# Kernel optimization log

Measured on AMD Instinct MI355X. Metric: run time of the kernel, lower is better.

## Reference

```python
import jax, jax.numpy as jnp
import numpy as np

N, H2, T = 64, 1024, 512  # num steps/documents, 2*hidden_dim, tokens per step
EPS = 1e-12  # torch F.normalize eps


def setup_inputs() -> dict:
    key = jax.random.key(0)
    k1, k2, k3, k4 = jax.random.split(key, 4)
    return {
        "hidden_states": jax.random.normal(k1, (N, H2, T), dtype=jnp.float32),
        "W_attention": jax.random.normal(k2, (H2, H2), dtype=jnp.float32),
        "bias_attention": jax.random.normal(k3, (H2,), dtype=jnp.float32),
        "u_w0": jax.random.normal(k4, (H2,), dtype=jnp.float32),
    }


def reference(hidden_states, W_attention, bias_attention, u_w0):
    n = hidden_states.shape[0]

    # Sequential recurrence on u_w: u_w <- normalize(u_w @ W^T + b), updated
    # BEFORE being used at each step i. Collect the post-update value per step.
    def step(u, _):
        u_new = u @ W_attention.T + bias_attention
        u_new = u_new / jnp.maximum(jnp.linalg.norm(u_new), EPS)
        return u_new, u_new

    _, u_ws = jax.lax.scan(step, u_w0, None, length=n)  # (N, 2H)

    # u_it = tanh(h_i^T W^T + b) for all steps, batched: (N, T, 2H)
    u_it = jnp.tanh(jnp.einsum('ndt,ed->nte', hidden_states, W_attention)
                    + bias_attention)

    # attention scores per step, softmax over the T axis (torch Softmax(dim=0)
    # on a (T,1) column)
    scores = jnp.einsum('nte,ne->nt', u_it, u_ws)  # (N, T)
    a = jax.nn.softmax(scores, axis=1)

    # weighted sum s_i = h_i @ a_i -> stacked as rows: (N, 2H)
    s = jnp.einsum('ndt,nt->nd', hidden_states, a)
    return s
```

## Files before the change

### kernel.cpp

```cpp
#include <hip/hip_runtime.h>
#include <cstdint>
#include <cstddef>

#define H2 1024
#define TT 512
#define NSTEPS 64
#define RBLK 32
#define RTHR 512
#define PREBLK 224
#define TOTBLK (RBLK + PREBLK)

using floatx4 = __attribute__((__ext_vector_type__(4))) float;
using half8   = __attribute__((__ext_vector_type__(8))) _Float16;
using half4   = __attribute__((__ext_vector_type__(4))) _Float16;
typedef unsigned long long u64;

__device__ __forceinline__ float tanh_fast(float x) {
  return 1.0f - 2.0f / (__expf(2.0f * x) + 1.0f);
}

#define GLDS16(gp, lp)                                                         \
  __builtin_amdgcn_global_load_lds(                                            \
      (const __attribute__((address_space(1))) void*)(gp),                     \
      (__attribute__((address_space(3))) void*)(lp), 16, 0, 0)

__global__ __launch_bounds__(RTHR, 1) void recur_pre_kernel(
    const float* __restrict__ W, const float* __restrict__ bias,
    const float* __restrict__ u0, float* __restrict__ vbuf,
    float* __restrict__ norm2, _Float16* __restrict__ Wh,
    const float* __restrict__ h, _Float16* __restrict__ hhT) {
  __shared__ __align__(16) char smem[2 * 16640];
  int tid = threadIdx.x;

  if (blockIdx.x < RBLK) {
    float* ub = (float*)smem;
    float* bredn = (float*)(smem + 8192);
    int w = tid >> 6, l = tid & 63;
    int r0 = blockIdx.x * RBLK + w * 4;

    floatx4 wreg[16];
    float blv[4];
#pragma unroll
    for (int p = 0; p < 4; ++p) {
      const float* wr = W + ((size_t)(r0 + p) << 10) + 4 * l;
#pragma unroll
      for (int j = 0; j < 4; ++j)
        wreg[p * 4 + j] = *(const floatx4*)(wr + 256 * j);
      blv[p] = bias[r0 + p];
    }
#pragma unroll
    for (int j = 0; j < 16; ++j) asm volatile("" : "+v"(wreg[j]));

    for (int i = 0; i < NSTEPS; ++i) {
      float* cb = ub + (i & 1) * 1024;
      float rs;
      if (i == 0) {
        if (w == 0) {
#pragma unroll
          for (int j = 0; j < 4; ++j) {
            floatx4 v = *((const floatx4*)u0 + l + 64 * j);
            *(floatx4*)(cb + 4 * l + 256 * j) = v;
          }
        }
        __syncthreads();
        rs = 1.0f;
      } else {
        if (w == 0) {
          const u64* src = (const u64*)(vbuf + ((size_t)(i - 1) << 10)) + l;
          u64 v[8];
          for (;;) {
            bool ok = true;
#pragma unroll
            for (int j = 0; j < 8; ++j) {
              v[j] = __hip_atomic_load(src + 64 * j, __ATOMIC_RELAXED,
                                       __HIP_MEMORY_SCOPE_AGENT);
              ok &= ((unsigned)(v[j] & 0xFFFFFFFFu) != 0xFFFFFFFFu) &
                    ((unsigned)(v[j] >> 32) != 0xFFFFFFFFu);
            }
            if (__all(ok)) break;
          }
          float sq = 0.f;
#pragma unroll
          for (int j = 0; j < 8; ++j) {
            *(u64*)(cb + 2 * l + 128 * j) = v[j];
            float f0 =
                __builtin_bit_cast(float, (unsigned)(v[j] & 0xFFFFFFFFu));
            float f1 = __builtin_bit_cast(float, (unsigned)(v[j] >> 32));
            sq += f0 * f0 + f1 * f1;
          }
#pragma unroll
          for (int off = 1; off <= 32; off <<= 1)
            sq += __shfl_xor(sq, off, 64);
          if (l == 0) bredn[i & 1] = sq;
        }
        __syncthreads();
        float nrm = bredn[i & 1];
        rs = 1.0f / fmaxf(sqrtf(nrm), 1e-12f);
        if (blockIdx.x == 0 && tid == 64) norm2[i - 1] = nrm;
      }

      float acc0 = 0.f, acc1 = 0.f, acc2 = 0.f, acc3 = 0.f;
#pragma unroll
      for (int j = 0; j < 4; ++j) {
        floatx4 zv = *(const floatx4*)(cb + 256 * j + 4 * l);
        floatx4 w0 = wreg[0 * 4 + j], w1 = wreg[1 * 4 + j];
        floatx4 w2 = wreg[2 * 4 + j], w3 = wreg[3 * 4 + j];
        acc0 += w0.x * zv.x + w0.y * zv.y + w0.z * zv.z + w0.w * zv.w;
        acc1 += w1.x * zv.x + w1.y * zv.y + w1.z * zv.z + w1.w * zv.w;
        acc2 += w2.x * zv.x + w2.y * zv.y + w2.z * zv.z + w2.w * zv.w;
        acc3 += w3.x * zv.x + w3.y * zv.y + w3.z * zv.z + w3.w * zv.w;
      }
#pragma unroll
      for (int off = 1; off <= 32; off <<= 1) {
        acc0 += __shfl_xor(acc0, off, 64);
        acc1 += __shfl_xor(acc1, off, 64);
        acc2 += __shfl_xor(acc2, off, 64);
        acc3 += __shfl_xor(acc3, off, 64);
      }
      if (l == 0) {
        float y0 = acc0 * rs + blv[0], y1 = acc1 * rs + blv[1];
        float y2 = acc2 * rs + blv[2], y3 = acc3 * rs + blv[3];
        u64 a01 = ((u64)__builtin_bit_cast(unsigned, y1) << 32) |
                  (u64)__builtin_bit_cast(unsigned, y0);
        u64 a23 = ((u64)__builtin_bit_cast(unsigned, y3) << 32) |
                  (u64)__builtin_bit_cast(unsigned, y2);
        u64* dst = (u64*)(vbuf + ((size_t)i << 10) + r0);
        __hip_atomic_store(dst, a01, __ATOMIC_RELAXED,
                           __HIP_MEMORY_SCOPE_AGENT);
        __hip_atomic_store(dst + 1, a23, __ATOMIC_RELAXED,
                           __HIP_MEMORY_SCOPE_AGENT);
      }
    }

    if (blockIdx.x == 0 && w == 0) {
      const u64* src = (const u64*)(vbuf + ((size_t)(NSTEPS - 1) << 10)) + l;
      u64 v[8];
      for (;;) {
        bool ok = true;
#pragma unroll
        for (int j = 0; j < 8; ++j) {
          v[j] = __hip_atomic_load(src + 64 * j, __ATOMIC_RELAXED,
                                   __HIP_MEMORY_SCOPE_AGENT);
          ok &= ((unsigned)(v[j] & 0xFFFFFFFFu) != 0xFFFFFFFFu) &
                ((unsigned)(v[j] >> 32) != 0xFFFFFFFFu);
        }
        if (__all(ok)) break;
      }
      float sq = 0.f;
#pragma unroll
      for (int j = 0; j < 8; ++j) {
        float f0 = __builtin_bit_cast(float, (unsigned)(v[j] & 0xFFFFFFFFu));
        float f1 = __builtin_bit_cast(float, (unsigned)(v[j] >> 32));
        sq += f0 * f0 + f1 * f1;
      }
#pragma unroll
      for (int off = 1; off <= 32; off <<= 1) sq += __shfl_xor(sq, off, 64);
      if (l == 0) norm2[NSTEPS - 1] = sq;
    }
  } else {
    int pb = blockIdx.x - RBLK;

    const floatx4* Wv = (const floatx4*)W;
    for (int idx = pb * RTHR + tid; idx < H2 * H2 / 4; idx += PREBLK * RTHR) {
      floatx4 v = Wv[idx];
      half4 o = {(_Float16)v.x, (_Float16)v.y, (_Float16)v.z, (_Float16)v.w};
      ((half4*)Wh)[idx] = o;
    }

    int sub = tid >> 8, ltid = tid & 255;
    float(*tile)[65] = (float(*)[65])(smem + sub * 16640);
    int dr = ltid >> 4, tc = (ltid & 15) << 2;
    int tr = ltid >> 3, seg = ltid & 7;
    for (int base = pb * 2; base < 8192; base += PREBLK * 2) {
      int tidx = base + sub;
      bool act = tidx < 8192;
      int n = tidx >> 7, rem = tidx & 127;
      int d0 = (rem & 15) << 6, t0 = ((rem >> 4) & 7) << 6;
      if (act) {
        const float* hb = h + ((size_t)n * H2 + d0) * TT + t0;
#pragma unroll
        for (int p = 0; p < 4; ++p) {
          floatx4 v = *(const floatx4*)(hb + (size_t)(dr + p * 16) * TT + tc);
          tile[dr + p * 16][tc] = v.x;
          tile[dr + p * 16][tc + 1] = v.y;
          tile[dr + p * 16][tc + 2] = v.z;
          tile[dr + p * 16][tc + 3] = v.w;
        }
      }
      __syncthreads();
      if (act) {
        _Float16* ob = hhT + ((size_t)n * TT + t0) * H2 + d0;
#pragma unroll
        for (int p = 0; p < 2; ++p) {
          int t = tr + p * 32;
          half8 hv;
#pragma unroll
          for (int u = 0; u < 8; ++u) hv[u] = (_Float16)tile[seg * 8 + u][t];
          *(half8*)(ob + (size_t)t * H2 + seg * 8) = hv;
        }
      }
      __syncthreads();
    }
  }
}

__global__ __launch_bounds__(256) void gemm2(
    const _Float16* __restrict__ Wh, const _Float16* __restrict__ hhT,
    const float* __restrict__ bias, const float* __restrict__ vbuf,
    const float* __restrict__ norm2, float* __restrict__ scores) {
  int x = blockIdx.x;
  int xcd = x & 7, slot = x >> 3;
  int e_t = slot & 7;
  int tn = xcd * 32 + (slot >> 3);
  int t_t = tn & 3, n = tn >> 2;
  int e_base = e_t * 128, t_base = t_t * 128;

  int tid = threadIdx.x, lane = tid & 63, w = tid >> 6;
  int q = lane >> 4, m = lane & 15;
  int eoff = (w & 1) * 64, toff = (w >> 1) * 64;

  __shared__ __align__(16) _Float16 Ash[128 * 32];
  __shared__ __align__(16) _Float16 Bsh[128 * 32];

  floatx4 zero = {0.f, 0.f, 0.f, 0.f};
  floatx4 acc[4][4];
#pragma unroll
  for (int i = 0; i < 4; ++i)
#pragma unroll
    for (int j = 0; j < 4; ++j) acc[i][j] = zero;

  int rl = lane >> 2, kseg = lane & 3;
  const _Float16* gA0 =
      Wh + (((size_t)(e_base + w * 32 + rl)) << 10) + kseg * 8;
  const _Float16* gA1 = gA0 + ((size_t)16 << 10);
  const _Float16* gB0 = hhT + ((size_t)n << 19) +
                        (((size_t)(t_base + w * 32 + rl)) << 10) + kseg * 8;
  const _Float16* gB1 = gB0 + ((size_t)16 << 10);
  _Float16* lA0 = Ash + (w * 32) * 32;
  _Float16* lA1 = lA0 + 16 * 32;
  _Float16* lB0 = Bsh + (w * 32) * 32;
  _Float16* lB1 = lB0 + 16 * 32;

  for (int k0 = 0; k0 < H2; k0 += 32) {
    GLDS16(gA0 + k0, lA0);
    GLDS16(gA1 + k0, lA1);
    GLDS16(gB0 + k0, lB0);
    GLDS16(gB1 + k0, lB1);
    __syncthreads();

    half8 af[4], bf[4];
#pragma unroll
    for (int i = 0; i < 4; ++i)
      af[i] = *(const half8*)&Ash[(eoff + i * 16 + m) * 32 + q * 8];
#pragma unroll
    for (int j = 0; j < 4; ++j)
      bf[j] = *(const half8*)&Bsh[(toff + j * 16 + m) * 32 + q * 8];
#pragma unroll
    for (int i = 0; i < 4; ++i)
#pragma unroll
      for (int j = 0; j < 4; ++j)
        acc[i][j] =
            __builtin_amdgcn_mfma_f32_16x16x32_f16(af[i], bf[j], acc[i][j], 0, 0, 0);
    __syncthreads();
  }

  float* uloc = (float*)Ash;
  float* bloc = uloc + 128;
  if (tid < 128) {
    float rsn = 1.0f / fmaxf(sqrtf(norm2[n]), 1e-12f);
    uloc[tid] = vbuf[((size_t)n << 10) + e_base + tid] * rsn;
    bloc[tid] = bias[e_base + tid];
  }
  __syncthreads();

  float part[4] = {0.f, 0.f, 0.f, 0.f};
#pragma unroll
  for (int i = 0; i < 4; ++i) {
#pragma unroll
    for (int reg = 0; reg < 4; ++reg) {
      int el = eoff + i * 16 + q * 4 + reg;
      float ubv = uloc[el];
      float bbv = bloc[el];
#pragma unroll
      for (int j = 0; j < 4; ++j) {
        float y = acc[i][j][reg] + bbv;
        part[j] += tanh_fast(y) * ubv;
      }
    }
  }
#pragma unroll
  for (int j = 0; j < 4; ++j) {
    part[j] += __shfl_xor(part[j], 16, 64);
    part[j] += __shfl_xor(part[j], 32, 64);
    if (lane < 16) {
      int t = t_base + toff + j * 16 + lane;
      atomicAdd(&scores[(size_t)n * TT + t], part[j]);
    }
  }
}

__global__ __launch_bounds__(256) void out_kernel(
    const float* __restrict__ h, const float* __restrict__ scores,
    float* __restrict__ out) {
  int n = blockIdx.y;
  int ds = blockIdx.x;
  int tid = threadIdx.x;
  int w = tid >> 6, lane = tid & 63;

  __shared__ float sa[TT];
  __shared__ float wred[8];

  float s0 = scores[(size_t)n * TT + tid];
  float s1 = scores[(size_t)n * TT + 256 + tid];

  float mx = fmaxf(s0, s1);
#pragma unroll
  for (int off = 32; off >= 1; off >>= 1) mx = fmaxf(mx, __shfl_xor(mx, off, 64));
  if (lane == 0) wred[w] = mx;
  __syncthreads();
  mx = fmaxf(fmaxf(wred[0], wred[1]), fmaxf(wred[2], wred[3]));

  float e0 = __expf(s0 - mx);
  float e1 = __expf(s1 - mx);
  float ssum = e0 + e1;
#pragma unroll
  for (int off = 32; off >= 1; off >>= 1) ssum += __shfl_xor(ssum, off, 64);
  if (lane == 0) wred[4 + w] = ssum;
  __syncthreads();
  ssum = wred[4] + wred[5] + wred[6] + wred[7];
  float inv = 1.0f / ssum;
  sa[tid] = e0 * inv;
  sa[tid + 256] = e1 * inv;
  __syncthreads();

  int d0 = ds * 64 + w * 16;
  const float4* hb = reinterpret_cast<const float4*>(h + (size_t)n * H2 * TT);
#pragma unroll 1
  for (int rr = 0; rr < 16; ++rr) {
    int d = d0 + rr;
    const float4* hr = hb + (size_t)d * (TT / 4);
    float4 a4 = hr[lane];
    float4 b4 = hr[64 + lane];
    int t0 = 4 * lane;
    float acc = a4.x * sa[t0] + a4.y * sa[t0 + 1] + a4.z * sa[t0 + 2] +
                a4.w * sa[t0 + 3] + b4.x * sa[256 + t0] +
                b4.y * sa[256 + t0 + 1] + b4.z * sa[256 + t0 + 2] +
                b4.w * sa[256 + t0 + 3];
#pragma unroll
    for (int off = 1; off <= 32; off <<= 1) acc += __shfl_xor(acc, off, 64);
    if (lane == 0) out[(size_t)n * H2 + d] = acc;
  }
}

extern "C" void kernel_launch(void* const* d_in, const int* in_sizes, int n_in,
                              void* d_out, int out_size, void* d_ws, size_t ws_size,
                              hipStream_t stream) {
  const float* h    = (const float*)d_in[0];
  const float* W    = (const float*)d_in[1];
  const float* bias = (const float*)d_in[2];
  const float* u0   = (const float*)d_in[3];
  float* out = (float*)d_out;

  float* wsf    = (float*)d_ws;
  float* norm2  = wsf;
  float* scores = wsf + 64;
  float* vbuf   = wsf + 64 + NSTEPS * TT;
  unsigned* ctr = (unsigned*)(vbuf + (size_t)NSTEPS * H2);
  float* after_ctr = (float*)(ctr + 16);
  _Float16* Wh  = (_Float16*)after_ctr;
  _Float16* hhT = Wh + (size_t)H2 * H2;

  hipMemsetAsync(d_ws, 0, (size_t)(64 + NSTEPS * TT) * sizeof(float), stream);
  hipMemsetAsync(vbuf, 0xFF, (size_t)NSTEPS * H2 * sizeof(float), stream);

  {
    const float* Wp = W; const float* bp = bias; const float* up = u0;
    float* vp = vbuf; float* np = norm2;
    _Float16* whp = Wh; const float* hp = h; _Float16* htp = hhT;
    void* kargs[] = {&Wp, &bp, &up, &vp, &np, &whp, &hp, &htp};
    hipLaunchCooperativeKernel((void*)recur_pre_kernel, dim3(TOTBLK),
                               dim3(RTHR), kargs, 0, stream);
  }

  gemm2<<<dim3(2048), dim3(256), 0, stream>>>(Wh, hhT, bias, vbuf, norm2,
                                              scores);
  out_kernel<<<dim3(16, 64), dim3(256), 0, stream>>>(h, scores, out);

  (void)in_sizes; (void)n_in; (void)out_size; (void)ws_size;
}
```

Before: 520.7 us.

## Fuse score GEMM into cooperative kernel with dynamic tile queue overlapping recurrence

Folds the separate gemm2 launch into the cooperative recurrence/preprocess kernel. Once all preprocessing blocks signal completion through a counter, all 256 blocks pull GEMM tiles from an atomic work queue, two tiles per 512-thread block. Each tile spin-waits on per-step sentinel values in norm2 and vbuf only at its epilogue, so the GEMM can overlap with the sequential u_w recurrence. This removes one kernel launch and the serialization between recurrence and GEMM. In exchange it adds spin polling, atomic stores for the fp16 conversions, and occupancy limited to the cooperative grid, and the recurrence blocks now share the device with GEMM work.

```diff
diff --git a/kernel.cpp b/kernel.cpp
--- a/kernel.cpp
+++ b/kernel.cpp
@@ -8,7 +8,8 @@
 #define RBLK 32
 #define RTHR 512
 #define PREBLK 224
-#define TOTBLK (RBLK + PREBLK)
+#define TOTBLK 256
+#define NTILES 2048u
 
 using floatx4 = __attribute__((__ext_vector_type__(4))) float;
 using half8   = __attribute__((__ext_vector_type__(8))) _Float16;
@@ -24,13 +25,16 @@
       (const __attribute__((address_space(1))) void*)(gp),                     \
       (__attribute__((address_space(3))) void*)(lp), 16, 0, 0)
 
-__global__ __launch_bounds__(RTHR, 1) void recur_pre_kernel(
+__global__ __launch_bounds__(RTHR, 1) void fused_kernel(
     const float* __restrict__ W, const float* __restrict__ bias,
     const float* __restrict__ u0, float* __restrict__ vbuf,
     float* __restrict__ norm2, _Float16* __restrict__ Wh,
-    const float* __restrict__ h, _Float16* __restrict__ hhT) {
-  __shared__ __align__(16) char smem[2 * 16640];
+    const float* __restrict__ h, _Float16* __restrict__ hhT,
+    float* __restrict__ scores, unsigned* __restrict__ ctrs) {
+  __shared__ __align__(16) char smem[33792];
   int tid = threadIdx.x;
+  unsigned* done  = ctrs;
+  unsigned* queue = ctrs + 16;
 
   if (blockIdx.x < RBLK) {
     float* ub = (float*)smem;
@@ -78,6 +82,7 @@
                     ((unsigned)(v[j] >> 32) != 0xFFFFFFFFu);
             }
             if (__all(ok)) break;
+            __builtin_amdgcn_s_sleep(1);
           }
           float sq = 0.f;
 #pragma unroll
@@ -96,7 +101,11 @@
         __syncthreads();
         float nrm = bredn[i & 1];
         rs = 1.0f / fmaxf(sqrtf(nrm), 1e-12f);
-        if (blockIdx.x == 0 && tid == 64) norm2[i - 1] = nrm;
+        if (blockIdx.x == 0 && tid == 64) {
+          unsigned nb = __builtin_bit_cast(unsigned, nrm);
+          __hip_atomic_store((unsigned*)(norm2 + (i - 1)), nb,
+                             __ATOMIC_RELAXED, __HIP_MEMORY_SCOPE_AGENT);
+        }
       }
 
       float acc0 = 0.f, acc1 = 0.f, acc2 = 0.f, acc3 = 0.f;
@@ -132,8 +141,9 @@
       }
     }
 
-    if (blockIdx.x == 0 && w == 0) {
-      const u64* src = (const u64*)(vbuf + ((size_t)(NSTEPS - 1) << 10)) + l;
+    if (blockIdx.x == 0 && (tid >> 6) == 0) {
+      int l2 = tid & 63;
+      const u64* src = (const u64*)(vbuf + ((size_t)(NSTEPS - 1) << 10)) + l2;
       u64 v[8];
       for (;;) {
         bool ok = true;
@@ -145,6 +155,7 @@
                 ((unsigned)(v[j] >> 32) != 0xFFFFFFFFu);
         }
         if (__all(ok)) break;
+        __builtin_amdgcn_s_sleep(1);
       }
       float sq = 0.f;
 #pragma unroll
@@ -155,8 +166,13 @@
       }
 #pragma unroll
       for (int off = 1; off <= 32; off <<= 1) sq += __shfl_xor(sq, off, 64);
-      if (l == 0) norm2[NSTEPS - 1] = sq;
-    }
+      if (l2 == 0) {
+        unsigned nb = __builtin_bit_cast(unsigned, sq);
+        __hip_atomic_store((unsigned*)(norm2 + (NSTEPS - 1)), nb,
+                           __ATOMIC_RELAXED, __HIP_MEMORY_SCOPE_AGENT);
+      }
+    }
+    __syncthreads();
   } else {
     int pb = blockIdx.x - RBLK;
 
@@ -164,7 +180,8 @@
     for (int idx = pb * RTHR + tid; idx < H2 * H2 / 4; idx += PREBLK * RTHR) {
       floatx4 v = Wv[idx];
       half4 o = {(_Float16)v.x, (_Float16)v.y, (_Float16)v.z, (_Float16)v.w};
-      ((half4*)Wh)[idx] = o;
+      __hip_atomic_store((u64*)Wh + idx, __builtin_bit_cast(u64, o),
+                         __ATOMIC_RELAXED, __HIP_MEMORY_SCOPE_AGENT);
     }
 
     int sub = tid >> 8, ltid = tid & 255;
@@ -193,109 +210,153 @@
 #pragma unroll
         for (int p = 0; p < 2; ++p) {
           int t = tr + p * 32;
-          half8 hv;
-#pragma unroll
-          for (int u = 0; u < 8; ++u) hv[u] = (_Float16)tile[seg * 8 + u][t];
-          *(half8*)(ob + (size_t)t * H2 + seg * 8) = hv;
+          union { half8 v; u64 u[2]; } hu;
+#pragma unroll
+          for (int u = 0; u < 8; ++u) hu.v[u] = (_Float16)tile[seg * 8 + u][t];
+          u64* op = (u64*)(ob + (size_t)t * H2 + seg * 8);
+          __hip_atomic_store(op, hu.u[0], __ATOMIC_RELAXED,
+                             __HIP_MEMORY_SCOPE_AGENT);
+          __hip_atomic_store(op + 1, hu.u[1], __ATOMIC_RELAXED,
+                             __HIP_MEMORY_SCOPE_AGENT);
         }
       }
       __syncthreads();
     }
+    asm volatile("s_waitcnt vmcnt(0)" ::: "memory");
+    __syncthreads();
+    if (tid == 0)
+      __hip_atomic_fetch_add(done, 1u, __ATOMIC_RELEASE,
+                             __HIP_MEMORY_SCOPE_AGENT);
   }
-}
-
-__global__ __launch_bounds__(256) void gemm2(
-    const _Float16* __restrict__ Wh, const _Float16* __restrict__ hhT,
-    const float* __restrict__ bias, const float* __restrict__ vbuf,
-    const float* __restrict__ norm2, float* __restrict__ scores) {
-  int x = blockIdx.x;
-  int xcd = x & 7, slot = x >> 3;
-  int e_t = slot & 7;
-  int tn = xcd * 32 + (slot >> 3);
-  int t_t = tn & 3, n = tn >> 2;
-  int e_base = e_t * 128, t_base = t_t * 128;
-
-  int tid = threadIdx.x, lane = tid & 63, w = tid >> 6;
-  int q = lane >> 4, m = lane & 15;
-  int eoff = (w & 1) * 64, toff = (w >> 1) * 64;
-
-  __shared__ __align__(16) _Float16 Ash[128 * 32];
-  __shared__ __align__(16) _Float16 Bsh[128 * 32];
-
-  floatx4 zero = {0.f, 0.f, 0.f, 0.f};
-  floatx4 acc[4][4];
-#pragma unroll
-  for (int i = 0; i < 4; ++i)
-#pragma unroll
-    for (int j = 0; j < 4; ++j) acc[i][j] = zero;
-
-  int rl = lane >> 2, kseg = lane & 3;
-  const _Float16* gA0 =
-      Wh + (((size_t)(e_base + w * 32 + rl)) << 10) + kseg * 8;
-  const _Float16* gA1 = gA0 + ((size_t)16 << 10);
-  const _Float16* gB0 = hhT + ((size_t)n << 19) +
-                        (((size_t)(t_base + w * 32 + rl)) << 10) + kseg * 8;
-  const _Float16* gB1 = gB0 + ((size_t)16 << 10);
-  _Float16* lA0 = Ash + (w * 32) * 32;
-  _Float16* lA1 = lA0 + 16 * 32;
-  _Float16* lB0 = Bsh + (w * 32) * 32;
-  _Float16* lB1 = lB0 + 16 * 32;
-
-  for (int k0 = 0; k0 < H2; k0 += 32) {
-    GLDS16(gA0 + k0, lA0);
-    GLDS16(gA1 + k0, lA1);
-    GLDS16(gB0 + k0, lB0);
-    GLDS16(gB1 + k0, lB1);
-    __syncthreads();
-
-    half8 af[4], bf[4];
-#pragma unroll
-    for (int i = 0; i < 4; ++i)
-      af[i] = *(const half8*)&Ash[(eoff + i * 16 + m) * 32 + q * 8];
-#pragma unroll
-    for (int j = 0; j < 4; ++j)
-      bf[j] = *(const half8*)&Bsh[(toff + j * 16 + m) * 32 + q * 8];
-#pragma unroll
-    for (int i = 0; i < 4; ++i)
-#pragma unroll
-      for (int j = 0; j < 4; ++j)
-        acc[i][j] =
-            __builtin_amdgcn_mfma_f32_16x16x32_f16(af[i], bf[j], acc[i][j], 0, 0, 0);
-    __syncthreads();
-  }
-
-  float* uloc = (float*)Ash;
-  float* bloc = uloc + 128;
-  if (tid < 128) {
-    float rsn = 1.0f / fmaxf(sqrtf(norm2[n]), 1e-12f);
-    uloc[tid] = vbuf[((size_t)n << 10) + e_base + tid] * rsn;
-    bloc[tid] = bias[e_base + tid];
+
+  if (tid == 0) {
+    while (__hip_atomic_load(done, __ATOMIC_ACQUIRE,
+                             __HIP_MEMORY_SCOPE_AGENT) < (unsigned)PREBLK)
+      __builtin_amdgcn_s_sleep(2);
   }
   __syncthreads();
 
-  float part[4] = {0.f, 0.f, 0.f, 0.f};
-#pragma unroll
-  for (int i = 0; i < 4; ++i) {
-#pragma unroll
-    for (int reg = 0; reg < 4; ++reg) {
-      int el = eoff + i * 16 + q * 4 + reg;
-      float ubv = uloc[el];
-      float bbv = bloc[el];
-#pragma unroll
-      for (int j = 0; j < 4; ++j) {
-        float y = acc[i][j][reg] + bbv;
-        part[j] += tanh_fast(y) * ubv;
-      }
-    }
-  }
-#pragma unroll
-  for (int j = 0; j < 4; ++j) {
-    part[j] += __shfl_xor(part[j], 16, 64);
-    part[j] += __shfl_xor(part[j], 32, 64);
-    if (lane < 16) {
-      int t = t_base + toff + j * 16 + lane;
-      atomicAdd(&scores[(size_t)n * TT + t], part[j]);
-    }
+  int half = tid >> 8, tid2 = tid & 255;
+  _Float16* Ash = (_Float16*)(smem + half * 16384);
+  _Float16* Bsh = Ash + 4096;
+  unsigned* tslot = (unsigned*)(smem + 32768);
+
+  int lane = tid2 & 63, w2 = tid2 >> 6;
+  int q = lane >> 4, m = lane & 15;
+  int eoff = (w2 & 1) * 64, toff = (w2 >> 1) * 64;
+  int rl = lane >> 2, kseg = lane & 3;
+  _Float16* lA0 = Ash + (w2 * 32) * 32;
+  _Float16* lA1 = lA0 + 16 * 32;
+  _Float16* lB0 = Bsh + (w2 * 32) * 32;
+  _Float16* lB1 = lB0 + 16 * 32;
+
+  for (;;) {
+    if (tid == 0) {
+      unsigned q0 = atomicAdd(queue, 2u);
+      tslot[0] = q0;
+      tslot[1] = q0 + 1u;
+    }
+    __syncthreads();
+    if (tslot[0] >= NTILES) break;
+    unsigned tau = tslot[half];
+    int n = (int)(tau >> 5);
+    int rem = (int)(tau & 31u);
+    int e_base = (rem & 7) << 7, t_base = (rem >> 3) << 7;
+
+    const _Float16* gA0 =
+        Wh + (((size_t)(e_base + w2 * 32 + rl)) << 10) + kseg * 8;
+    const _Float16* gA1 = gA0 + ((size_t)16 << 10);
+    const _Float16* gB0 = hhT + ((size_t)n << 19) +
+                          (((size_t)(t_base + w2 * 32 + rl)) << 10) + kseg * 8;
+    const _Float16* gB1 = gB0 + ((size_t)16 << 10);
+
+    floatx4 zero = {0.f, 0.f, 0.f, 0.f};
+    floatx4 acc[4][4];
+#pragma unroll
+    for (int i = 0; i < 4; ++i)
+#pragma unroll
+      for (int j = 0; j < 4; ++j) acc[i][j] = zero;
+
+    for (int k0 = 0; k0 < H2; k0 += 32) {
+      GLDS16(gA0 + k0, lA0);
+      GLDS16(gA1 + k0, lA1);
+      GLDS16(gB0 + k0, lB0);
+      GLDS16(gB1 + k0, lB1);
+      __syncthreads();
+
+      half8 af[4], bf[4];
+#pragma unroll
+      for (int i = 0; i < 4; ++i)
+        af[i] = *(const half8*)&Ash[(eoff + i * 16 + m) * 32 + q * 8];
+#pragma unroll
+      for (int j = 0; j < 4; ++j)
+        bf[j] = *(const half8*)&Bsh[(toff + j * 16 + m) * 32 + q * 8];
+#pragma unroll
+      for (int i = 0; i < 4; ++i)
+#pragma unroll
+        for (int j = 0; j < 4; ++j)
+          acc[i][j] = __builtin_amdgcn_mfma_f32_16x16x32_f16(af[i], bf[j],
+                                                             acc[i][j], 0, 0, 0);
+      __syncthreads();
+    }
+
+    float* uloc = (float*)Ash;
+    float* bloc = uloc + 128;
+    if (tid2 < 128) {
+      float nn;
+      for (;;) {
+        unsigned b = __hip_atomic_load((const unsigned*)(norm2 + n),
+                                       __ATOMIC_RELAXED,
+                                       __HIP_MEMORY_SCOPE_AGENT);
+        if (b != 0xFFFFFFFFu) {
+          nn = __builtin_bit_cast(float, b);
+          break;
+        }
+        __builtin_amdgcn_s_sleep(1);
+      }
+      float rsn = 1.0f / fmaxf(sqrtf(nn), 1e-12f);
+      const unsigned* vp =
+          (const unsigned*)(vbuf + ((size_t)n << 10) + e_base) + tid2;
+      float vv;
+      for (;;) {
+        unsigned b =
+            __hip_atomic_load(vp, __ATOMIC_RELAXED, __HIP_MEMORY_SCOPE_AGENT);
+        if (b != 0xFFFFFFFFu) {
+          vv = __builtin_bit_cast(float, b);
+          break;
+        }
+        __builtin_amdgcn_s_sleep(1);
+      }
+      uloc[tid2] = vv * rsn;
+      bloc[tid2] = bias[e_base + tid2];
+    }
+    __syncthreads();
+
+    float part[4] = {0.f, 0.f, 0.f, 0.f};
+#pragma unroll
+    for (int i = 0; i < 4; ++i) {
+#pragma unroll
+      for (int reg = 0; reg < 4; ++reg) {
+        int el = eoff + i * 16 + q * 4 + reg;
+        float ubv = uloc[el];
+        float bbv = bloc[el];
+#pragma unroll
+        for (int j = 0; j < 4; ++j) {
+          float y = acc[i][j][reg] + bbv;
+          part[j] += tanh_fast(y) * ubv;
+        }
+      }
+    }
+#pragma unroll
+    for (int j = 0; j < 4; ++j) {
+      part[j] += __shfl_xor(part[j], 16, 64);
+      part[j] += __shfl_xor(part[j], 32, 64);
+      if (lane < 16) {
+        int t = t_base + toff + j * 16 + lane;
+        atomicAdd(&scores[(size_t)n * TT + t], part[j]);
+      }
+    }
+    __syncthreads();
   }
 }
 
@@ -365,25 +426,26 @@
   float* norm2  = wsf;
   float* scores = wsf + 64;
   float* vbuf   = wsf + 64 + NSTEPS * TT;
-  unsigned* ctr = (unsigned*)(vbuf + (size_t)NSTEPS * H2);
-  float* after_ctr = (float*)(ctr + 16);
-  _Float16* Wh  = (_Float16*)after_ctr;
+  unsigned* ctrs = (unsigned*)(vbuf + (size_t)NSTEPS * H2);
+  float* after = (float*)(ctrs + 32);
+  _Float16* Wh  = (_Float16*)after;
   _Float16* hhT = Wh + (size_t)H2 * H2;
 
-  hipMemsetAsync(d_ws, 0, (size_t)(64 + NSTEPS * TT) * sizeof(float), stream);
+  hipMemsetAsync(norm2, 0xFF, 64 * sizeof(float), stream);
+  hipMemsetAsync(scores, 0, (size_t)NSTEPS * TT * sizeof(float), stream);
   hipMemsetAsync(vbuf, 0xFF, (size_t)NSTEPS * H2 * sizeof(float), stream);
+  hipMemsetAsync(ctrs, 0, 32 * sizeof(unsigned), stream);
 
   {
     const float* Wp = W; const float* bp = bias; const float* up = u0;
     float* vp = vbuf; float* np = norm2;
     _Float16* whp = Wh; const float* hp = h; _Float16* htp = hhT;
-    void* kargs[] = {&Wp, &bp, &up, &vp, &np, &whp, &hp, &htp};
-    hipLaunchCooperativeKernel((void*)recur_pre_kernel, dim3(TOTBLK),
-                               dim3(RTHR), kargs, 0, stream);
+    float* sp = scores; unsigned* cp = ctrs;
+    void* kargs[] = {&Wp, &bp, &up, &vp, &np, &whp, &hp, &htp, &sp, &cp};
+    hipLaunchCooperativeKernel((void*)fused_kernel, dim3(TOTBLK), dim3(RTHR),
+                               kargs, 0, stream);
   }
 
-  gemm2<<<dim3(2048), dim3(256), 0, stream>>>(Wh, hhT, bias, vbuf, norm2,
-                                              scores);
   out_kernel<<<dim3(16, 64), dim3(256), 0, stream>>>(h, scores, out);
 
   (void)in_sizes; (void)n_in; (void)out_size; (void)ws_size;
```

Measured after the change: 489.1 us. 1.06x faster.
